# Optimization experiments

Hardware: AMD Instinct MI355X
Metric: run time of the kernel (lower is better)

Reference implementation:

```python
import jax, jax.numpy as jnp
import numpy as np

N = 131072      # total nodes
B = 16          # graphs in batch (num_segments)
C = 128         # in_channels
K = 16          # n_super_nodes
TAU = 1.0
PRUNING_THRESHOLD = 0.01
SPARSITY_WEIGHT = 0.01
TEMPORAL_W = 0.1 * 5
COLLAPSE_W = 2.0
EPS = 1e-9


def setup_inputs() -> dict:
    key = jax.random.key(0)
    ks = jax.random.split(key, 8)
    x = jax.random.normal(ks[0], (N, C), dtype=jnp.float32)
    batch = jnp.sort(jax.random.randint(ks[1], (N,), 0, B)).astype(jnp.int64)
    pos = jax.random.normal(ks[2], (N, 2), dtype=jnp.float32)
    # Gumbel noise for gumbel_softmax (sampled once, passed as input for determinism)
    gumbel = jax.random.gumbel(ks[3], (N, K), dtype=jnp.float32)
    # assign_mlp params: Linear(C,C) -> ReLU -> Linear(C,K)
    W1 = jax.random.normal(ks[4], (C, C), dtype=jnp.float32) / np.sqrt(C)
    b1 = jnp.zeros((C,), dtype=jnp.float32)
    W2 = jax.random.normal(ks[5], (K, C), dtype=jnp.float32) / np.sqrt(C)
    b2 = jnp.zeros((K,), dtype=jnp.float32)
    scaling = jnp.asarray(10.0, dtype=jnp.float32)
    active_mask = jnp.ones((K,), dtype=jnp.float32)  # buffer, starts all-active
    return {"x": x, "batch": batch, "pos": pos, "gumbel": gumbel,
            "W1": W1, "b1": b1, "W2": W2, "b2": b2,
            "scaling": scaling, "active_mask": active_mask}


def reference(x, batch, pos, gumbel, W1, b1, W2, b2, scaling, active_mask):
    # --- assignment logits: MLP * scaling (eval mode, prev_assignments=None) ---
    h = jax.nn.relu(x @ W1.T + b1)            # [N, C]
    logits = (h @ W2.T + b2) * scaling        # [N, K]
    # eval-path masking: masked_fill(mask == 0, -1e9)
    masked_logits = jnp.where(active_mask[None, :] == 0.0, -1e9, logits)
    # gumbel_softmax (soft, hard=False)
    s = jax.nn.softmax((masked_logits + gumbel) / TAU, axis=-1)   # [N, K]

    avg_s = jnp.mean(s, axis=0)               # [K]

    # --- losses ---
    entropy = -jnp.mean(jnp.sum(s * jnp.log(s + EPS), axis=1))
    uniform_p = 1.0 / K
    diversity = jnp.sum(uniform_p * jnp.log(uniform_p / (avg_s + EPS)))
    pruning = jnp.mean(jnp.abs(avg_s * (1.0 - active_mask)))
    sparsity = (jnp.sum(active_mask) / K) * SPARSITY_WEIGHT
    temporal = jnp.asarray(0.0, jnp.float32)  # prev_assignments is None
    # collapse-prevention / balance bodies are truncated upstream; faithful proxies
    collapse = jnp.sum((avg_s - uniform_p) ** 2) * COLLAPSE_W
    balance = jnp.std(avg_s)
    spatial = jnp.asarray(0.0, jnp.float32)

    # --- pooled features: out[b,k,c] = sum_{n in graph b} s[n,k] * x[n,c] ---
    weighted = x[:, None, :] * s[:, :, None]                  # [N, K, C]
    out = jax.ops.segment_sum(weighted, batch, num_segments=B)  # [B, K, C]

    # --- super-node positions ---
    w_pos = pos[:, None, :] * s[:, :, None]                    # [N, K, 2]
    sum_s_pos = jax.ops.segment_sum(w_pos, batch, num_segments=B)  # [B, K, 2]
    sum_s = jax.ops.segment_sum(s, batch, num_segments=B)[..., None] + EPS  # [B, K, 1]
    mu = sum_s_pos / sum_s                                     # [B, K, 2]

    # --- separation loss: pairwise repulsion between super-node centers ---
    dist_sq = jnp.sum((mu[:, :, None, :] - mu[:, None, :, :]) ** 2, axis=-1)  # [B,K,K]
    eye = jnp.eye(K, dtype=mu.dtype)[None]
    repulsion = 1.0 / (dist_sq + 1.0)
    separation = jnp.sum(repulsion * (1.0 - eye)) / (K * (K - 1))

    losses = jnp.stack([entropy, diversity, spatial, pruning, sparsity,
                        temporal * TEMPORAL_W, collapse, balance, separation])
    return out, s, mu, losses
```

## Files before the change

### kernel.cpp

```cpp
#include <hip/hip_runtime.h>
#include <hip/hip_bf16.h>
#include <math.h>

#define NN 131072
#define BSEG 16
#define CCH 128
#define KK 16
#define EPSF 1e-9f
#define XST 136

#define OFF_S   32768
#define OFF_MU  2129920
#define OFF_L   2130432

#define REDC_BASE 1024
#define REDC_STRIDE 1024
#define NRED 64
#define ST_BASE (REDC_BASE + NRED * REDC_STRIDE)
#define NST 4
#define ST_SZ (BSEG * KK * CCH)

#define TILES 2

typedef __bf16 bf16x8 __attribute__((ext_vector_type(8)));
typedef float  f32x4  __attribute__((ext_vector_type(4)));
typedef float  f32x16 __attribute__((ext_vector_type(16)));

__device__ __forceinline__ int load_batch(const void* bptr, int n, int is64) {
    if (is64) return (int)((const long long*)bptr)[n];
    return ((const int*)bptr)[n];
}

__device__ __forceinline__ float wave_sum(float v) {
#pragma unroll
    for (int o = 32; o > 0; o >>= 1) v += __shfl_xor(v, o, 64);
    return v;
}

__device__ __forceinline__ bf16x8 pack8(float4 a, float4 b) {
    bf16x8 v;
    v[0] = (__bf16)a.x; v[1] = (__bf16)a.y; v[2] = (__bf16)a.z; v[3] = (__bf16)a.w;
    v[4] = (__bf16)b.x; v[5] = (__bf16)b.y; v[6] = (__bf16)b.z; v[7] = (__bf16)b.w;
    return v;
}

__global__ void k_zero(float* __restrict__ ws, const int* __restrict__ b32) {
    int i = blockIdx.x * 256 + threadIdx.x;
    ws[REDC_BASE + i] = 0.0f;
    if (i == 0) ws[0] = (b32[NN - 1] == 0) ? 1.0f : 0.0f;
}

__global__ __launch_bounds__(256, 2) void k_fused(
    const float* __restrict__ x, const void* __restrict__ batch,
    const float* __restrict__ pos, const float* __restrict__ gumbel,
    const float* __restrict__ W1, const float* __restrict__ b1,
    const float* __restrict__ W2, const float* __restrict__ b2,
    const float* __restrict__ scaling, const float* __restrict__ active_mask,
    float* __restrict__ s_out, float* __restrict__ ws)
{
    __shared__ __align__(16) __bf16 x_lds[128 * XST];
    __shared__ __align__(16) __bf16 h_lds[128 * XST];
    __shared__ __align__(16) __bf16 sT[16 * XST];
    __shared__ float2 pos_lds[128];
    __shared__ int bsegs[128];

    const int tid  = threadIdx.x;
    const int lane = tid & 63;
    const int wv   = tid >> 6;
    const int is64 = (int)ws[0];

    float* rc  = ws + REDC_BASE + (size_t)(blockIdx.x & (NRED - 1)) * REDC_STRIDE;
    float* stg = ws + ST_BASE   + (size_t)(blockIdx.x & (NST  - 1)) * ST_SZ;

    bf16x8 bfr[8];
    {
        const float* wrow = W1 + (size_t)(wv * 32 + (lane & 31)) * CCH + (lane >> 5) * 8;
#pragma unroll
        for (int ks = 0; ks < 8; ks++) {
            float4 u = *(const float4*)(wrow + ks * 16);
            float4 v = *(const float4*)(wrow + ks * 16 + 4);
            bfr[ks] = pack8(u, v);
        }
    }
    const float b1j = b1[wv * 32 + (lane & 31)];

    f32x4 pacc[2];
#pragma unroll
    for (int t = 0; t < 2; t++)
#pragma unroll
        for (int r = 0; r < 4; r++) pacc[t][r] = 0.0f;
    int curseg = -1;

    for (int t = 0; t < TILES; t++) {
        const int n0 = blockIdx.x * (TILES * 128) + t * 128;

        if (t) __syncthreads();

        if (tid < 128) {
            bsegs[tid] = load_batch(batch, n0 + tid, is64);
            pos_lds[tid] = ((const float2*)pos)[n0 + tid];
        }
        float gu[2][4];
        {
            const int g  = lane >> 4;
            const int kq = lane & 15;
#pragma unroll
            for (int tt = 0; tt < 2; tt++)
#pragma unroll
                for (int r = 0; r < 4; r++) {
                    int node = (wv * 2 + tt) * 16 + g * 4 + r;
                    gu[tt][r] = gumbel[(size_t)(n0 + node) * KK + kq];
                }
        }
        {
            const float4* xg = (const float4*)(x + (size_t)n0 * CCH);
#pragma unroll
            for (int i = 0; i < 8; i++) {
                int p = i * 256 + tid;
                float4 a = xg[2 * p], b = xg[2 * p + 1];
                *(bf16x8*)&x_lds[(p >> 4) * XST + (p & 15) * 8] = pack8(a, b);
            }
        }
        __syncthreads();

        {
            f32x16 acc[4];
#pragma unroll
            for (int mt = 0; mt < 4; mt++)
#pragma unroll
                for (int r = 0; r < 16; r++) acc[mt][r] = 0.0f;

#pragma unroll
            for (int ks = 0; ks < 8; ks++) {
#pragma unroll
                for (int mt = 0; mt < 4; mt++) {
                    bf16x8 a = *(bf16x8*)&x_lds[(size_t)(mt * 32 + (lane & 31)) * XST + ks * 16 + (lane >> 5) * 8];
                    acc[mt] = __builtin_amdgcn_mfma_f32_32x32x16_bf16(a, bfr[ks], acc[mt], 0, 0, 0);
                }
            }
#pragma unroll
            for (int mt = 0; mt < 4; mt++)
#pragma unroll
                for (int r = 0; r < 16; r++) {
                    int node = mt * 32 + (r & 3) + 8 * (r >> 2) + 4 * (lane >> 5);
                    h_lds[(size_t)node * XST + wv * 32 + (lane & 31)] = (__bf16)fmaxf(acc[mt][r] + b1j, 0.0f);
                }
        }
        __syncthreads();

        {
            const int g  = lane >> 4;
            const int kq = lane & 15;
            const int bf = bsegs[0], bl = bsegs[127];

            const float b2k = b2[kq];
            const float amk = active_mask[kq];
            const float sc  = scaling[0];

            f32x4 acc2[2];
#pragma unroll
            for (int tt = 0; tt < 2; tt++)
#pragma unroll
                for (int r = 0; r < 4; r++) acc2[tt][r] = 0.0f;

#pragma unroll
            for (int ks = 0; ks < 4; ks++) {
                const float* w2row = W2 + (size_t)kq * CCH + ks * 32 + g * 8;
                float4 u = *(const float4*)w2row;
                float4 v4 = *(const float4*)(w2row + 4);
                bf16x8 bwf = pack8(u, v4);
#pragma unroll
                for (int tt = 0; tt < 2; tt++) {
                    bf16x8 a = *(bf16x8*)&h_lds[(size_t)((wv * 2 + tt) * 16 + kq) * XST + ks * 32 + g * 8];
                    acc2[tt] = __builtin_amdgcn_mfma_f32_16x16x32_bf16(a, bwf, acc2[tt], 0, 0, 0);
                }
            }

            float saccA = 0.f, pxA = 0.f, pyA = 0.f;
            float saccB = 0.f, pxB = 0.f, pyB = 0.f;
            float entacc = 0.f;
            const bool dual = (bf != bl);

#pragma unroll
            for (int tt = 0; tt < 2; tt++) {
#pragma unroll
                for (int r = 0; r < 4; r++) {
                    const int node = (wv * 2 + tt) * 16 + g * 4 + r;
                    float v = (acc2[tt][r] + b2k) * sc;
                    if (amk == 0.0f) v = -1e9f;
                    v += gu[tt][r];
                    float m = v;
#pragma unroll
                    for (int o = 1; o < 16; o <<= 1) m = fmaxf(m, __shfl_xor(m, o, 64));
                    float e = expf(v - m);
                    float ssum = e;
#pragma unroll
                    for (int o = 1; o < 16; o <<= 1) ssum += __shfl_xor(ssum, o, 64);
                    float s = e / ssum;

                    s_out[(size_t)(n0 + node) * KK + kq] = s;
                    sT[kq * XST + node] = (__bf16)s;

                    float te = s * logf(s + EPSF);
#pragma unroll
                    for (int o = 1; o < 16; o <<= 1) te += __shfl_xor(te, o, 64);
                    entacc += te;

                    const float2 pp = pos_lds[node];
                    const float w0 = (bsegs[node] == bf) ? 1.0f : 0.0f;
                    const float sA = s * w0;
                    saccA += sA; pxA += sA * pp.x; pyA += sA * pp.y;
                    if (dual) {
                        const float sB = s - sA;
                        saccB += sB; pxB += sB * pp.x; pyB += sB * pp.y;
                    }
                }
            }

            saccA += __shfl_xor(saccA, 16, 64); saccA += __shfl_xor(saccA, 32, 64);
            pxA   += __shfl_xor(pxA,   16, 64); pxA   += __shfl_xor(pxA,   32, 64);
            pyA   += __shfl_xor(pyA,   16, 64); pyA   += __shfl_xor(pyA,   32, 64);
            if (lane < 16) {
                atomicAdd(&rc[bf * 16 + lane], saccA);
                atomicAdd(&rc[256 + bf * 32 + 2 * lane],     pxA);
                atomicAdd(&rc[256 + bf * 32 + 2 * lane + 1], pyA);
            }
            if (dual) {
                saccB += __shfl_xor(saccB, 16, 64); saccB += __shfl_xor(saccB, 32, 64);
                pxB   += __shfl_xor(pxB,   16, 64); pxB   += __shfl_xor(pxB,   32, 64);
                pyB   += __shfl_xor(pyB,   16, 64); pyB   += __shfl_xor(pyB,   32, 64);
                if (lane < 16) {
                    atomicAdd(&rc[bl * 16 + lane], saccB);
                    atomicAdd(&rc[256 + bl * 32 + 2 * lane],     pxB);
                    atomicAdd(&rc[256 + bl * 32 + 2 * lane + 1], pyB);
                }
            }
            float entw = wave_sum(entacc);
            if (lane == 0) atomicAdd(&rc[768], entw * 0.0625f);
        }
        __syncthreads();

        {
            const int bf = bsegs[0], bl = bsegs[127];
            const bool masked = (bf != bl);
            for (int seg = bf; seg <= bl; seg++) {
                if (seg != curseg) {
                    if (curseg >= 0) {
#pragma unroll
                        for (int tt = 0; tt < 2; tt++) {
#pragma unroll
                            for (int r = 0; r < 4; r++) {
                                int k = (lane >> 4) * 4 + r;
                                int c = (wv * 2 + tt) * 16 + (lane & 15);
                                atomicAdd(&stg[((size_t)curseg * KK + k) * CCH + c], pacc[tt][r]);
                            }
#pragma unroll
                            for (int r = 0; r < 4; r++) pacc[tt][r] = 0.0f;
                        }
                    }
                    curseg = seg;
                }
#pragma unroll
                for (int ks = 0; ks < 4; ks++) {
                    bf16x8 a = *(bf16x8*)&sT[(size_t)(lane & 15) * XST + ks * 32 + (lane >> 4) * 8];
                    if (masked) {
#pragma unroll
                        for (int i = 0; i < 8; i++) {
                            int nd = ks * 32 + (lane >> 4) * 8 + i;
                            if (bsegs[nd] != seg) a[i] = (__bf16)0.0f;
                        }
                    }
#pragma unroll
                    for (int tt = 0; tt < 2; tt++) {
                        int ct = wv * 2 + tt;
                        bf16x8 bx;
#pragma unroll
                        for (int i = 0; i < 8; i++)
                            bx[i] = x_lds[(size_t)(ks * 32 + (lane >> 4) * 8 + i) * XST + ct * 16 + (lane & 15)];
                        pacc[tt] = __builtin_amdgcn_mfma_f32_16x16x32_bf16(a, bx, pacc[tt], 0, 0, 0);
                    }
                }
            }
        }
    }

    if (curseg >= 0) {
#pragma unroll
        for (int tt = 0; tt < 2; tt++) {
#pragma unroll
            for (int r = 0; r < 4; r++) {
                int k = (lane >> 4) * 4 + r;
                int c = (wv * 2 + tt) * 16 + (lane & 15);
                atomicAdd(&stg[((size_t)curseg * KK + k) * CCH + c], pacc[tt][r]);
            }
        }
    }
}

__global__ __launch_bounds__(256) void k_tail(
    const float* __restrict__ ws, const float* __restrict__ active_mask,
    float* __restrict__ out, float* __restrict__ mu_out, float* __restrict__ losses)
{
    const int tid = threadIdx.x;

    if (blockIdx.x < 32) {
        int i = blockIdx.x * 256 + tid;
        const float4* s0 = (const float4*)(ws + ST_BASE);
        const float4* s1 = (const float4*)(ws + ST_BASE + ST_SZ);
        const float4* s2 = (const float4*)(ws + ST_BASE + 2 * ST_SZ);
        const float4* s3 = (const float4*)(ws + ST_BASE + 3 * ST_SZ);
        float4 a = s0[i], b = s1[i], c = s2[i], d = s3[i];
        float4 r;
        r.x = (a.x + b.x) + (c.x + d.x);
        r.y = (a.y + b.y) + (c.y + d.y);
        r.z = (a.z + b.z) + (c.z + d.z);
        r.w = (a.w + b.w) + (c.w + d.w);
        ((float4*)out)[i] = r;
        return;
    }

    __shared__ float lsum[256];
    __shared__ float lpos[512];
    __shared__ float lent[1];
    __shared__ float smu[512];
    __shared__ float savg[16];
    __shared__ float red[256];

    for (int a = tid; a < 769; a += 256) {
        float acc = 0.0f;
#pragma unroll 8
        for (int c = 0; c < NRED; c++) acc += ws[REDC_BASE + c * REDC_STRIDE + a];
        if (a < 256) lsum[a] = acc;
        else if (a < 768) lpos[a - 256] = acc;
        else lent[0] = acc;
    }
    __syncthreads();

    if (tid < 16) {
        float a = 0.0f;
#pragma unroll
        for (int b = 0; b < 16; b++) a += lsum[b * 16 + tid];
        savg[tid] = a / (float)NN;
    }
    for (int i = tid; i < 512; i += 256) {
        int sk = i >> 1;
        float v = lpos[i] / (lsum[sk] + EPSF);
        smu[i] = v;
        mu_out[i] = v;
    }
    __syncthreads();

    float rep = 0.0f;
    for (int t = tid; t < 4096; t += 256) {
        int b = t >> 8, i = (t >> 4) & 15, j = t & 15;
        if (i != j) {
            float dx = smu[b * 32 + i * 2]     - smu[b * 32 + j * 2];
            float dy = smu[b * 32 + i * 2 + 1] - smu[b * 32 + j * 2 + 1];
            rep += 1.0f / (dx * dx + dy * dy + 1.0f);
        }
    }
    red[tid] = rep;
    __syncthreads();
    for (int st = 128; st > 0; st >>= 1) {
        if (tid < st) red[tid] += red[tid + st];
        __syncthreads();
    }

    if (tid == 0) {
        const float p = 1.0f / 16.0f;
        float separation = red[0] / (float)(16 * 15);
        float entropy = -lent[0] / (float)NN;
        float diversity = 0.f, pruning = 0.f, amsum = 0.f, collapse = 0.f, mean = 0.f;
        for (int k = 0; k < 16; k++) {
            float a = savg[k];
            diversity += p * logf(p / (a + EPSF));
            pruning += fabsf(a * (1.0f - active_mask[k]));
            amsum += active_mask[k];
            collapse += (a - p) * (a - p);
            mean += a;
        }
        pruning /= 16.0f;
        mean /= 16.0f;
        float var = 0.f;
        for (int k = 0; k < 16; k++) { float d = savg[k] - mean; var += d * d; }
        float balance = sqrtf(var / 16.0f);
        float sparsity = (amsum / 16.0f) * 0.01f;
        collapse *= 2.0f;
        losses[0] = entropy;   losses[1] = diversity; losses[2] = 0.0f;
        losses[3] = pruning;   losses[4] = sparsity;  losses[5] = 0.0f;
        losses[6] = collapse;  losses[7] = balance;   losses[8] = separation;
    }
}

extern "C" void kernel_launch(void* const* d_in, const int* in_sizes, int n_in,
                              void* d_out, int out_size, void* d_ws, size_t ws_size,
                              hipStream_t stream) {
    const float* x       = (const float*)d_in[0];
    const void*  batch   = d_in[1];
    const float* pos     = (const float*)d_in[2];
    const float* gumbel  = (const float*)d_in[3];
    const float* W1      = (const float*)d_in[4];
    const float* b1      = (const float*)d_in[5];
    const float* W2      = (const float*)d_in[6];
    const float* b2      = (const float*)d_in[7];
    const float* scaling = (const float*)d_in[8];
    const float* am      = (const float*)d_in[9];

    float* out      = (float*)d_out;
    float* s_sec    = out + OFF_S;
    float* mu_sec   = out + OFF_MU;
    float* loss_sec = out + OFF_L;
    float* wsf      = (float*)d_ws;

    k_zero<<<768, 256, 0, stream>>>(wsf, (const int*)batch);
    k_fused<<<NN / 256, 256, 0, stream>>>(x, batch, pos, gumbel, W1, b1, W2, b2,
                                          scaling, am, s_sec, wsf);
    k_tail<<<33, 256, 0, stream>>>(wsf, am, out, mu_sec, loss_sec);
}
```

Measured before the change: 156.3 us.

## Transpose logits MFMA so each lane owns a node row, doubling staging copies

Swaps the operands of the second MFMA so the logits come out transposed: each lane holds four consecutive super-node values for one node. The softmax then needs only two cross-lane shuffles instead of sixteen-lane butterflies, and gumbel loads and s stores become float4 vector accesses. Entropy is accumulated per node without the per-k shuffle reduction. Separately, the number of staging copies for the pooled-output atomics doubles from 4 to 8, which spreads atomic contention at the cost of more zeroing and a larger tail reduction.

```diff
diff --git a/kernel.cpp b/kernel.cpp
--- a/kernel.cpp
+++ b/kernel.cpp
@@ -17,7 +17,7 @@
 #define REDC_STRIDE 1024
 #define NRED 64
 #define ST_BASE (REDC_BASE + NRED * REDC_STRIDE)
-#define NST 4
+#define NST 8
 #define ST_SZ (BSEG * KK * CCH)
 
 #define TILES 2
@@ -100,17 +100,15 @@
             bsegs[tid] = load_batch(batch, n0 + tid, is64);
             pos_lds[tid] = ((const float2*)pos)[n0 + tid];
         }
-        float gu[2][4];
+        const int nd = lane & 15;
+        const int g  = lane >> 4;
+        float4 gu[2];
         {
-            const int g  = lane >> 4;
-            const int kq = lane & 15;
-#pragma unroll
-            for (int tt = 0; tt < 2; tt++)
-#pragma unroll
-                for (int r = 0; r < 4; r++) {
-                    int node = (wv * 2 + tt) * 16 + g * 4 + r;
-                    gu[tt][r] = gumbel[(size_t)(n0 + node) * KK + kq];
-                }
+#pragma unroll
+            for (int tt = 0; tt < 2; tt++) {
+                int node = (wv * 2 + tt) * 16 + nd;
+                gu[tt] = *(const float4*)(gumbel + (size_t)(n0 + node) * KK + g * 4);
+            }
         }
         {
             const float4* xg = (const float4*)(x + (size_t)n0 * CCH);
@@ -149,13 +147,11 @@
         __syncthreads();
 
         {
-            const int g  = lane >> 4;
-            const int kq = lane & 15;
             const int bf = bsegs[0], bl = bsegs[127];
-
-            const float b2k = b2[kq];
-            const float amk = active_mask[kq];
-            const float sc  = scaling[0];
+            const float sc = scaling[0];
+            float b2v[4], amv[4];
+#pragma unroll
+            for (int r = 0; r < 4; r++) { b2v[r] = b2[g * 4 + r]; amv[r] = active_mask[g * 4 + r]; }
 
             f32x4 acc2[2];
 #pragma unroll
@@ -165,78 +161,110 @@
 
 #pragma unroll
             for (int ks = 0; ks < 4; ks++) {
-                const float* w2row = W2 + (size_t)kq * CCH + ks * 32 + g * 8;
+                const float* w2row = W2 + (size_t)nd * CCH + ks * 32 + g * 8;
                 float4 u = *(const float4*)w2row;
                 float4 v4 = *(const float4*)(w2row + 4);
                 bf16x8 bwf = pack8(u, v4);
 #pragma unroll
                 for (int tt = 0; tt < 2; tt++) {
-                    bf16x8 a = *(bf16x8*)&h_lds[(size_t)((wv * 2 + tt) * 16 + kq) * XST + ks * 32 + g * 8];
-                    acc2[tt] = __builtin_amdgcn_mfma_f32_16x16x32_bf16(a, bwf, acc2[tt], 0, 0, 0);
-                }
-            }
-
-            float saccA = 0.f, pxA = 0.f, pyA = 0.f;
-            float saccB = 0.f, pxB = 0.f, pyB = 0.f;
-            float entacc = 0.f;
+                    bf16x8 a = *(bf16x8*)&h_lds[(size_t)((wv * 2 + tt) * 16 + nd) * XST + ks * 32 + g * 8];
+                    acc2[tt] = __builtin_amdgcn_mfma_f32_16x16x32_bf16(bwf, a, acc2[tt], 0, 0, 0);
+                }
+            }
+
+            float sA[4] = {0, 0, 0, 0}, pxA[4] = {0, 0, 0, 0}, pyA[4] = {0, 0, 0, 0};
+            float sB[4] = {0, 0, 0, 0}, pxB[4] = {0, 0, 0, 0}, pyB[4] = {0, 0, 0, 0};
+            float entacc = 0.0f;
             const bool dual = (bf != bl);
 
 #pragma unroll
             for (int tt = 0; tt < 2; tt++) {
+                const int node = (wv * 2 + tt) * 16 + nd;
+                float v[4];
 #pragma unroll
                 for (int r = 0; r < 4; r++) {
-                    const int node = (wv * 2 + tt) * 16 + g * 4 + r;
-                    float v = (acc2[tt][r] + b2k) * sc;
-                    if (amk == 0.0f) v = -1e9f;
-                    v += gu[tt][r];
-                    float m = v;
-#pragma unroll
-                    for (int o = 1; o < 16; o <<= 1) m = fmaxf(m, __shfl_xor(m, o, 64));
-                    float e = expf(v - m);
-                    float ssum = e;
-#pragma unroll
-                    for (int o = 1; o < 16; o <<= 1) ssum += __shfl_xor(ssum, o, 64);
-                    float s = e / ssum;
-
-                    s_out[(size_t)(n0 + node) * KK + kq] = s;
-                    sT[kq * XST + node] = (__bf16)s;
-
-                    float te = s * logf(s + EPSF);
-#pragma unroll
-                    for (int o = 1; o < 16; o <<= 1) te += __shfl_xor(te, o, 64);
-                    entacc += te;
-
-                    const float2 pp = pos_lds[node];
-                    const float w0 = (bsegs[node] == bf) ? 1.0f : 0.0f;
-                    const float sA = s * w0;
-                    saccA += sA; pxA += sA * pp.x; pyA += sA * pp.y;
-                    if (dual) {
-                        const float sB = s - sA;
-                        saccB += sB; pxB += sB * pp.x; pyB += sB * pp.y;
-                    }
-                }
-            }
-
-            saccA += __shfl_xor(saccA, 16, 64); saccA += __shfl_xor(saccA, 32, 64);
-            pxA   += __shfl_xor(pxA,   16, 64); pxA   += __shfl_xor(pxA,   32, 64);
-            pyA   += __shfl_xor(pyA,   16, 64); pyA   += __shfl_xor(pyA,   32, 64);
-            if (lane < 16) {
-                atomicAdd(&rc[bf * 16 + lane], saccA);
-                atomicAdd(&rc[256 + bf * 32 + 2 * lane],     pxA);
-                atomicAdd(&rc[256 + bf * 32 + 2 * lane + 1], pyA);
+                    float vv = (acc2[tt][r] + b2v[r]) * sc;
+                    if (amv[r] == 0.0f) vv = -1e9f;
+                    v[r] = vv + ((const float*)&gu[tt])[r];
+                }
+                float vm = fmaxf(fmaxf(v[0], v[1]), fmaxf(v[2], v[3]));
+                vm = fmaxf(vm, __shfl_xor(vm, 16, 64));
+                vm = fmaxf(vm, __shfl_xor(vm, 32, 64));
+                float e[4];
+                float ls = 0.0f;
+#pragma unroll
+                for (int r = 0; r < 4; r++) { e[r] = expf(v[r] - vm); ls += e[r]; }
+                ls += __shfl_xor(ls, 16, 64);
+                ls += __shfl_xor(ls, 32, 64);
+                const float inv = 1.0f / ls;
+                float s[4];
+#pragma unroll
+                for (int r = 0; r < 4; r++) s[r] = e[r] * inv;
+
+                float4 so; so.x = s[0]; so.y = s[1]; so.z = s[2]; so.w = s[3];
+                *(float4*)(s_out + (size_t)(n0 + node) * KK + g * 4) = so;
+#pragma unroll
+                for (int r = 0; r < 4; r++) sT[(g * 4 + r) * XST + node] = (__bf16)s[r];
+
+#pragma unroll
+                for (int r = 0; r < 4; r++) entacc += s[r] * logf(s[r] + EPSF);
+
+                const float2 pp = pos_lds[node];
+                const float w0 = (bsegs[node] == bf) ? 1.0f : 0.0f;
+#pragma unroll
+                for (int r = 0; r < 4; r++) {
+                    const float sa = s[r] * w0;
+                    sA[r] += sa; pxA[r] += sa * pp.x; pyA[r] += sa * pp.y;
+                }
+                if (dual) {
+#pragma unroll
+                    for (int r = 0; r < 4; r++) {
+                        const float sb = s[r] * (1.0f - w0);
+                        sB[r] += sb; pxB[r] += sb * pp.x; pyB[r] += sb * pp.y;
+                    }
+                }
+            }
+
+#pragma unroll
+            for (int o = 1; o < 16; o <<= 1) {
+#pragma unroll
+                for (int r = 0; r < 4; r++) {
+                    sA[r]  += __shfl_xor(sA[r],  o, 64);
+                    pxA[r] += __shfl_xor(pxA[r], o, 64);
+                    pyA[r] += __shfl_xor(pyA[r], o, 64);
+                }
+            }
+            if (nd == 0) {
+#pragma unroll
+                for (int r = 0; r < 4; r++) {
+                    const int k = g * 4 + r;
+                    atomicAdd(&rc[bf * 16 + k], sA[r]);
+                    atomicAdd(&rc[256 + bf * 32 + 2 * k],     pxA[r]);
+                    atomicAdd(&rc[256 + bf * 32 + 2 * k + 1], pyA[r]);
+                }
             }
             if (dual) {
-                saccB += __shfl_xor(saccB, 16, 64); saccB += __shfl_xor(saccB, 32, 64);
-                pxB   += __shfl_xor(pxB,   16, 64); pxB   += __shfl_xor(pxB,   32, 64);
-                pyB   += __shfl_xor(pyB,   16, 64); pyB   += __shfl_xor(pyB,   32, 64);
-                if (lane < 16) {
-                    atomicAdd(&rc[bl * 16 + lane], saccB);
-                    atomicAdd(&rc[256 + bl * 32 + 2 * lane],     pxB);
-                    atomicAdd(&rc[256 + bl * 32 + 2 * lane + 1], pyB);
+#pragma unroll
+                for (int o = 1; o < 16; o <<= 1) {
+#pragma unroll
+                    for (int r = 0; r < 4; r++) {
+                        sB[r]  += __shfl_xor(sB[r],  o, 64);
+                        pxB[r] += __shfl_xor(pxB[r], o, 64);
+                        pyB[r] += __shfl_xor(pyB[r], o, 64);
+                    }
+                }
+                if (nd == 0) {
+#pragma unroll
+                    for (int r = 0; r < 4; r++) {
+                        const int k = g * 4 + r;
+                        atomicAdd(&rc[bl * 16 + k], sB[r]);
+                        atomicAdd(&rc[256 + bl * 32 + 2 * k],     pxB[r]);
+                        atomicAdd(&rc[256 + bl * 32 + 2 * k + 1], pyB[r]);
+                    }
                 }
             }
             float entw = wave_sum(entacc);
-            if (lane == 0) atomicAdd(&rc[768], entw * 0.0625f);
+            if (lane == 0) atomicAdd(&rc[768], entw);
         }
         __syncthreads();
 
@@ -266,8 +294,8 @@
                     if (masked) {
 #pragma unroll
                         for (int i = 0; i < 8; i++) {
-                            int nd = ks * 32 + (lane >> 4) * 8 + i;
-                            if (bsegs[nd] != seg) a[i] = (__bf16)0.0f;
+                            int ndd = ks * 32 + (lane >> 4) * 8 + i;
+                            if (bsegs[ndd] != seg) a[i] = (__bf16)0.0f;
                         }
                     }
 #pragma unroll
@@ -305,16 +333,12 @@
 
     if (blockIdx.x < 32) {
         int i = blockIdx.x * 256 + tid;
-        const float4* s0 = (const float4*)(ws + ST_BASE);
-        const float4* s1 = (const float4*)(ws + ST_BASE + ST_SZ);
-        const float4* s2 = (const float4*)(ws + ST_BASE + 2 * ST_SZ);
-        const float4* s3 = (const float4*)(ws + ST_BASE + 3 * ST_SZ);
-        float4 a = s0[i], b = s1[i], c = s2[i], d = s3[i];
-        float4 r;
-        r.x = (a.x + b.x) + (c.x + d.x);
-        r.y = (a.y + b.y) + (c.y + d.y);
-        r.z = (a.z + b.z) + (c.z + d.z);
-        r.w = (a.w + b.w) + (c.w + d.w);
+        float4 r = make_float4(0.f, 0.f, 0.f, 0.f);
+#pragma unroll
+        for (int c = 0; c < NST; c++) {
+            float4 a = ((const float4*)(ws + ST_BASE + (size_t)c * ST_SZ))[i];
+            r.x += a.x; r.y += a.y; r.z += a.z; r.w += a.w;
+        }
         ((float4*)out)[i] = r;
         return;
     }
@@ -412,7 +436,7 @@
     float* loss_sec = out + OFF_L;
     float* wsf      = (float*)d_ws;
 
-    k_zero<<<768, 256, 0, stream>>>(wsf, (const int*)batch);
+    k_zero<<<1280, 256, 0, stream>>>(wsf, (const int*)batch);
     k_fused<<<NN / 256, 256, 0, stream>>>(x, batch, pos, gumbel, W1, b1, W2, b2,
                                           scaling, am, s_sec, wsf);
     k_tail<<<33, 256, 0, stream>>>(wsf, am, out, mu_sec, loss_sec);
```

Result: no change. 156.7 us (+0.2%).
